# Performance work log

Hardware: AMD Instinct MI355X
Metric: run time of the kernel (lower is better)

Reference implementation:

```python
import jax, jax.numpy as jnp
import numpy as np

B, S, D = 8, 1024, 1024
H, DK, DV = 16, 64, 64
MAXREL = 32
VOCAB = 2 * MAXREL + 1  # use_neg_dist=True


def setup_inputs() -> dict:
    key = jax.random.key(0)
    ks = jax.random.split(key, 16)
    s = 0.02
    return {
        "key": jax.random.normal(ks[0], (B, S, D), jnp.float32),
        "value": jax.random.normal(ks[1], (B, S, D), jnp.float32),
        "query": jax.random.normal(ks[2], (B, S, D), jnp.float32),
        # True = masked (masked_fill semantics)
        "mask": jax.random.bernoulli(ks[3], 0.1, (B, S, S)),
        # adjacency weights in {0,1,2}; 0 => disconnected, >0 => 1/adj reweight
        "adj_mask": jax.random.randint(ks[4], (B, H, S, S), 0, 3).astype(jnp.float32),
        "Wq": jax.random.normal(ks[5], (D, H * DK), jnp.float32) * s,
        "bq": jnp.zeros((H * DK,), jnp.float32),
        "Wk": jax.random.normal(ks[6], (D, H * DK), jnp.float32) * s,
        "bk": jnp.zeros((H * DK,), jnp.float32),
        "Wv": jax.random.normal(ks[7], (D, H * DV), jnp.float32) * s,
        "bv": jnp.zeros((H * DV,), jnp.float32),
        "Wo": jax.random.normal(ks[8], (H * DV, D), jnp.float32) * s,
        "bo": jnp.zeros((D,), jnp.float32),
        "rel_k": jax.random.normal(ks[9], (VOCAB, DK), jnp.float32) * s,
        "rel_v": jax.random.normal(ks[10], (VOCAB, DV), jnp.float32) * s,
    }


def reference(key, value, query, mask, adj_mask, Wq, bq, Wk, bk, Wv, bv, Wo, bo, rel_k, rel_v):
    Bq, Sq, _ = query.shape
    # project and split heads -> [B, H, S, d]
    k = (key @ Wk + bk).reshape(Bq, -1, H, DK).transpose(0, 2, 1, 3)
    q = (query @ Wq + bq).reshape(Bq, -1, H, DK).transpose(0, 2, 1, 3)
    v = (value @ Wv + bv).reshape(Bq, -1, H, DV).transpose(0, 2, 1, 3)
    Sk = k.shape[2]
    # relative position matrix (clamped signed distances, shifted to [0, 2*MAXREL])
    r = jnp.arange(Sk)
    dist = jnp.clip(r[None, :] - r[:, None], -MAXREL, MAXREL) + MAXREL  # [S, S]
    rk = rel_k[dist]  # [S, S, DK]
    rv = rel_v[dist]  # [S, S, DV]
    q = q / jnp.sqrt(jnp.asarray(DK, q.dtype))
    # content scores + relative-key scores (relative_matmul transpose=True)
    scores = jnp.einsum("bhqd,bhkd->bhqk", q, k) + jnp.einsum("bhqd,qkd->bhqk", q, rk)
    scores = scores.astype(jnp.float32)
    scores = jnp.where(mask[:, None, :, :], -1e18, scores)
    adj_b = adj_mask != 0.0
    scores = jnp.where(adj_b, scores, -1e18)
    attn = jax.nn.softmax(scores, axis=-1).astype(q.dtype)
    # adjacency renormalization: attn / adj where adj>0, then L1 normalize
    inv_adj = 1.0 / jnp.where(adj_b, adj_mask, 1e18)
    attn = attn * inv_adj
    attn = attn / jnp.maximum(jnp.sum(jnp.abs(attn), axis=-1, keepdims=True), 1e-12)
    # context + relative-value term (relative_matmul transpose=False)
    ctx = jnp.einsum("bhqk,bhkd->bhqd", attn, v) + jnp.einsum("bhqk,qkd->bhqd", attn, rv)
    ctx = ctx.transpose(0, 2, 1, 3).reshape(Bq, Sq, H * DV)
    final_output = ctx @ Wo + bo
    return final_output, attn
```

## Files before the change

### kernel.cpp

```cpp
#include <hip/hip_runtime.h>

typedef unsigned short u16;
typedef unsigned int u32;
typedef __bf16 bf16x8 __attribute__((ext_vector_type(8)));
typedef u16 u16x8 __attribute__((ext_vector_type(8)));
typedef float floatx4 __attribute__((ext_vector_type(4)));

#define B_ 8
#define S_ 1024
#define D_ 1024
#define H_ 16
#define NREL 65

__device__ __forceinline__ float b2f(u16 u) { return __uint_as_float(((u32)u) << 16); }
__device__ __forceinline__ u16 f2b(float f) {
    u32 x = __float_as_uint(f);
    x += 0x7fffu + ((x >> 16) & 1u);
    return (u16)(x >> 16);
}

__global__ __launch_bounds__(256) void transpose_w(const float* __restrict__ in,
                                                   u16* __restrict__ out) {
    __shared__ u16 tile[32][33];
    int c0 = blockIdx.x * 32, r0 = blockIdx.y * 32;
    int tx = threadIdx.x & 31, ty = threadIdx.x >> 5;
#pragma unroll
    for (int i = 0; i < 32; i += 8)
        tile[ty + i][tx] = f2b(in[(size_t)(r0 + ty + i) * 1024 + c0 + tx]);
    __syncthreads();
#pragma unroll
    for (int i = 0; i < 32; i += 8)
        out[(size_t)(c0 + ty + i) * 1024 + r0 + tx] = tile[tx][ty + i];
}

__global__ __launch_bounds__(256) void transpose_v(const u16* __restrict__ in,
                                                   u16* __restrict__ out) {
    __shared__ u16 tile[32][33];
    int bh = blockIdx.z;
    int s0 = blockIdx.x * 32, d0 = blockIdx.y * 32;
    int tx = threadIdx.x & 31, ty = threadIdx.x >> 5;
    const u16* ib = in + (size_t)bh * S_ * 64;
    u16* ob = out + (size_t)bh * S_ * 64;
#pragma unroll
    for (int i = 0; i < 32; i += 8)
        tile[ty + i][tx] = ib[(size_t)(s0 + ty + i) * 64 + d0 + tx];
    __syncthreads();
#pragma unroll
    for (int i = 0; i < 32; i += 8)
        ob[(size_t)(d0 + ty + i) * 1024 + s0 + tx] = tile[tx][ty + i];
}

__global__ __launch_bounds__(256, 2) void gemm_bt(
    const void* __restrict__ Av, const u16* __restrict__ WT, const float* __restrict__ bias,
    float* __restrict__ outf, u16* __restrict__ outb, int M, int K, int mode, int a_bf16,
    float scale) {
    __shared__ __align__(16) u16 As[128 * 64];
    __shared__ __align__(16) u16 Bs[128 * 64];
    int tid = threadIdx.x;
    int wave = tid >> 6, lane = tid & 63;
    int wm = (wave >> 1) * 64, wn = (wave & 1) * 64;
    int m0 = blockIdx.y * 128, n0 = blockIdx.x * 128;
    floatx4 acc[4][4] = {};
    for (int kt = 0; kt < K; kt += 64) {
        if (a_bf16) {
            const u16* A = (const u16*)Av;
#pragma unroll
            for (int i = 0; i < 4; i++) {
                int L = tid + 256 * i;
                int row = L >> 3, seg = (L & 7) * 8;
                *(uint4*)(As + row * 64 + seg) = *(const uint4*)(A + (size_t)(m0 + row) * K + kt + seg);
            }
        } else {
            const float* A = (const float*)Av;
#pragma unroll
            for (int i = 0; i < 8; i++) {
                int L = tid + 256 * i;
                int row = L >> 4, seg = (L & 15) * 4;
                float4 a = *(const float4*)(A + (size_t)(m0 + row) * K + kt + seg);
                ushort4 b;
                b.x = f2b(a.x); b.y = f2b(a.y); b.z = f2b(a.z); b.w = f2b(a.w);
                *(ushort4*)(As + row * 64 + seg) = b;
            }
        }
#pragma unroll
        for (int i = 0; i < 4; i++) {
            int L = tid + 256 * i;
            int row = L >> 3, seg = (L & 7) * 8;
            *(uint4*)(Bs + row * 64 + seg) = *(const uint4*)(WT + (size_t)(n0 + row) * K + kt + seg);
        }
        __syncthreads();
        int kb = (lane >> 4) * 8;
#pragma unroll
        for (int half = 0; half < 2; half++) {
            bf16x8 af[4], bfv[4];
#pragma unroll
            for (int mi = 0; mi < 4; mi++)
                af[mi] = *(const bf16x8*)(As + (wm + mi * 16 + (lane & 15)) * 64 + half * 32 + kb);
#pragma unroll
            for (int ni = 0; ni < 4; ni++)
                bfv[ni] = *(const bf16x8*)(Bs + (wn + ni * 16 + (lane & 15)) * 64 + half * 32 + kb);
#pragma unroll
            for (int mi = 0; mi < 4; mi++)
#pragma unroll
                for (int ni = 0; ni < 4; ni++)
                    acc[mi][ni] = __builtin_amdgcn_mfma_f32_16x16x32_bf16(af[mi], bfv[ni], acc[mi][ni], 0, 0, 0);
        }
        __syncthreads();
    }
    int lr = (lane >> 4) * 4, lc = lane & 15;
#pragma unroll
    for (int mi = 0; mi < 4; mi++) {
#pragma unroll
        for (int ni = 0; ni < 4; ni++) {
            int col = n0 + wn + ni * 16 + lc;
            float bv = bias[col];
#pragma unroll
            for (int r = 0; r < 4; r++) {
                int row = m0 + wm + mi * 16 + lr + r;
                float v = (acc[mi][ni][r] + bv) * scale;
                if (mode == 0) {
                    outf[(size_t)row * 1024 + col] = v;
                } else {
                    int b = row >> 10, s = row & 1023;
                    int hh = col >> 6, d = col & 63;
                    outb[(((size_t)(b * H_ + hh)) * S_ + s) * 64 + d] = f2b(v);
                }
            }
        }
    }
}

__global__ __launch_bounds__(256, 2) void attn_fused(
    const u16* __restrict__ qw, const u16* __restrict__ kw, const u16* __restrict__ vt,
    const int* __restrict__ mask, const float* __restrict__ adj,
    const float* __restrict__ relk, const float* __restrict__ relv,
    float* __restrict__ attn_out, u16* __restrict__ ctx) {
    __shared__ __align__(16) u16 s_attn[16 * 1024];
    __shared__ float s_qrel[16 * NREL];
    __shared__ float s_arel[16 * NREL];
    __shared__ float s_redm[4 * 16];
    __shared__ float s_reds[4 * 16 * 2];

    const int tid = threadIdx.x;
    const int w = tid >> 6;
    const int lane = tid & 63;
    const int g = lane >> 4;
    const int li = lane & 15;
    const int q0 = blockIdx.x * 16;
    const int h = blockIdx.y, b = blockIdx.z;
    const size_t bh = (size_t)b * H_ + h;
    const u16* qb = qw + bh * S_ * 64;
    const u16* kb = kw + bh * S_ * 64;

    bf16x8 aq[2];
#pragma unroll
    for (int kf = 0; kf < 2; kf++)
        aq[kf] = *(const bf16x8*)(qb + (size_t)(q0 + li) * 64 + kf * 32 + g * 8);

    for (int ni = w; ni < 5; ni += 4) {
        floatx4 qacc = {};
        int v = ni * 16 + li;
        int vc = v > 64 ? 64 : v;
#pragma unroll
        for (int kf = 0; kf < 2; kf++) {
            const float* rp = relk + vc * 64 + kf * 32 + g * 8;
            float4 f0 = *(const float4*)(rp);
            float4 f1 = *(const float4*)(rp + 4);
            u16x8 t;
            t[0] = f2b(f0.x); t[1] = f2b(f0.y); t[2] = f2b(f0.z); t[3] = f2b(f0.w);
            t[4] = f2b(f1.x); t[5] = f2b(f1.y); t[6] = f2b(f1.z); t[7] = f2b(f1.w);
            qacc = __builtin_amdgcn_mfma_f32_16x16x32_bf16(aq[kf], *(bf16x8*)&t, qacc, 0, 0, 0);
        }
        if (v <= 64) {
#pragma unroll
            for (int r = 0; r < 4; r++) s_qrel[(g * 4 + r) * NREL + v] = qacc[r];
        }
    }
    __syncthreads();

    floatx4 acc[16] = {};
#pragma unroll
    for (int kf = 0; kf < 2; kf++) {
#pragma unroll
        for (int ni = 0; ni < 16; ni++) {
            int kcol = w * 256 + ni * 16 + li;
            bf16x8 bk = *(const bf16x8*)(kb + (size_t)kcol * 64 + kf * 32 + g * 8);
            acc[ni] = __builtin_amdgcn_mfma_f32_16x16x32_bf16(aq[kf], bk, acc[ni], 0, 0, 0);
        }
    }

    const int* mbase = mask + (size_t)b * S_ * S_;
    const float* abase = adj + bh * S_ * S_;
#pragma unroll
    for (int ni = 0; ni < 16; ni++) {
        int kcol = w * 256 + ni * 16 + li;
#pragma unroll
        for (int r = 0; r < 4; r++) {
            int qpos = q0 + g * 4 + r;
            int dd = kcol - qpos;
            dd = max(-32, min(32, dd));
            float sc = acc[ni][r] + s_qrel[(g * 4 + r) * NREL + dd + 32];
            int mk = mbase[(size_t)qpos * S_ + kcol];
            float aj = abase[(size_t)qpos * S_ + kcol];
            if (mk != 0 || aj == 0.f) sc = -1e18f;
            acc[ni][r] = sc;
        }
    }

    float mr[4];
#pragma unroll
    for (int r = 0; r < 4; r++) {
        float m = acc[0][r];
#pragma unroll
        for (int ni = 1; ni < 16; ni++) m = fmaxf(m, acc[ni][r]);
#pragma unroll
        for (int o = 8; o > 0; o >>= 1) m = fmaxf(m, __shfl_xor(m, o, 16));
        mr[r] = m;
    }
    if (li == 0) {
#pragma unroll
        for (int r = 0; r < 4; r++) s_redm[w * 16 + g * 4 + r] = mr[r];
    }
    __syncthreads();
#pragma unroll
    for (int r = 0; r < 4; r++) {
        float m = s_redm[g * 4 + r];
#pragma unroll
        for (int ww = 1; ww < 4; ww++) m = fmaxf(m, s_redm[ww * 16 + g * 4 + r]);
        mr[r] = m;
    }

    float psum[4] = {0.f, 0.f, 0.f, 0.f}, pisum[4] = {0.f, 0.f, 0.f, 0.f};
#pragma unroll
    for (int ni = 0; ni < 16; ni++) {
        int kcol = w * 256 + ni * 16 + li;
#pragma unroll
        for (int r = 0; r < 4; r++) {
            int qpos = q0 + g * 4 + r;
            float aj = abase[(size_t)qpos * S_ + kcol];
            float p = __expf(acc[ni][r] - mr[r]);
            float inv = (aj != 0.f) ? (1.f / aj) : 1e-18f;
            float pi = p * inv;
            acc[ni][r] = pi;
            psum[r] += p;
            pisum[r] += pi;
        }
    }
#pragma unroll
    for (int r = 0; r < 4; r++)
#pragma unroll
        for (int o = 8; o > 0; o >>= 1) {
            psum[r] += __shfl_xor(psum[r], o, 16);
            pisum[r] += __shfl_xor(pisum[r], o, 16);
        }
    if (li == 0) {
#pragma unroll
        for (int r = 0; r < 4; r++) {
            s_reds[(w * 16 + g * 4 + r) * 2 + 0] = psum[r];
            s_reds[(w * 16 + g * 4 + r) * 2 + 1] = pisum[r];
        }
    }
    __syncthreads();
    float rden[4];
#pragma unroll
    for (int r = 0; r < 4; r++) {
        float ps = 0.f, pis = 0.f;
#pragma unroll
        for (int ww = 0; ww < 4; ww++) {
            ps += s_reds[(ww * 16 + g * 4 + r) * 2 + 0];
            pis += s_reds[(ww * 16 + g * 4 + r) * 2 + 1];
        }
        rden[r] = 1.f / fmaxf(pis, 1e-12f * ps);
    }

    float* ob = attn_out + bh * (size_t)S_ * S_;
#pragma unroll
    for (int ni = 0; ni < 16; ni++) {
        int kcol = w * 256 + ni * 16 + li;
#pragma unroll
        for (int r = 0; r < 4; r++) {
            int row = g * 4 + r;
            float at = acc[ni][r] * rden[r];
            ob[(size_t)(q0 + row) * S_ + kcol] = at;
            int byteoff = (row * 2048 + kcol * 2) ^ ((row & 7) << 4);
            *(u16*)((char*)s_attn + byteoff) = f2b(at);
        }
    }
    __syncthreads();

    {
        const int row = tid >> 4, sub = tid & 15;
        const int qpos = q0 + row;
        auto rd = [&](int k) -> float {
            int byteoff = (row * 2048 + k * 2) ^ ((row & 7) << 4);
            return b2f(*(const u16*)((const char*)s_attn + byteoff));
        };
        float s0v = 0.f;
        for (int k = sub; k <= qpos - 32; k += 16) s0v += rd(k);
#pragma unroll
        for (int o = 8; o > 0; o >>= 1) s0v += __shfl_xor(s0v, o, 16);
        if (sub == 0) s_arel[row * NREL + 0] = s0v;
        float s1v = 0.f;
        for (int k = qpos + 32 + sub; k < S_; k += 16) s1v += rd(k);
#pragma unroll
        for (int o = 8; o > 0; o >>= 1) s1v += __shfl_xor(s1v, o, 16);
        if (sub == 0) s_arel[row * NREL + 64] = s1v;
        for (int i = sub; i < 63; i += 16) {
            int v = 1 + i;
            int k = qpos + v - 32;
            s_arel[row * NREL + v] = (k >= 0 && k < S_) ? rd(k) : 0.f;
        }
    }

    floatx4 pv = {};
    const int d = w * 16 + li;
    const u16* vrow = vt + (bh * 64 + d) * (size_t)S_;
#pragma unroll 8
    for (int kt = 0; kt < S_; kt += 32) {
        int byteoff = (li * 2048 + (kt + g * 8) * 2) ^ ((li & 7) << 4);
        bf16x8 pa = *(const bf16x8*)((const char*)s_attn + byteoff);
        bf16x8 vb8 = *(const bf16x8*)(vrow + kt + g * 8);
        pv = __builtin_amdgcn_mfma_f32_16x16x32_bf16(pa, vb8, pv, 0, 0, 0);
    }
    __syncthreads();

#pragma unroll 1
    for (int v = 0; v < NREL; v++) {
        float rv = relv[v * 64 + d];
#pragma unroll
        for (int r = 0; r < 4; r++) pv[r] += s_arel[(g * 4 + r) * NREL + v] * rv;
    }
    u16* cb = ctx + ((size_t)b * S_ + q0) * 1024 + h * 64 + d;
#pragma unroll
    for (int r = 0; r < 4; r++) cb[(size_t)(g * 4 + r) * 1024] = f2b(pv[r]);
}

extern "C" void kernel_launch(void* const* d_in, const int* in_sizes, int n_in,
                              void* d_out, int out_size, void* d_ws, size_t ws_size,
                              hipStream_t stream) {
    const float* key   = (const float*)d_in[0];
    const float* value = (const float*)d_in[1];
    const float* query = (const float*)d_in[2];
    const int* mask    = (const int*)d_in[3];
    const float* adj   = (const float*)d_in[4];
    const float* Wq = (const float*)d_in[5];  const float* bq = (const float*)d_in[6];
    const float* Wk = (const float*)d_in[7];  const float* bk = (const float*)d_in[8];
    const float* Wv = (const float*)d_in[9];  const float* bv = (const float*)d_in[10];
    const float* Wo = (const float*)d_in[11]; const float* bo = (const float*)d_in[12];
    const float* relk = (const float*)d_in[13];
    const float* relv = (const float*)d_in[14];

    float* out_final = (float*)d_out;
    float* out_attn  = out_final + (size_t)B_ * S_ * D_;

    char* ws = (char*)d_ws;
    u16* wt  = (u16*)ws;
    u16* qws = (u16*)(ws + ((size_t)2 << 20));
    u16* kws = (u16*)(ws + ((size_t)18 << 20));
    u16* vws = (u16*)(ws + ((size_t)34 << 20));
    u16* vtw = (u16*)(ws + ((size_t)50 << 20));
    u16* cws = (u16*)(ws + ((size_t)66 << 20));

    dim3 tg(32, 32), tb(256);
    dim3 gg(8, 64), gb(256);
    dim3 vg(32, 2, 128), vb_(256);
    dim3 ag(64, 16, 8), ab(256);

    transpose_w<<<tg, tb, 0, stream>>>(Wq, wt);
    gemm_bt<<<gg, gb, 0, stream>>>(query, wt, bq, nullptr, qws, 8192, 1024, 1, 0, 0.125f);
    transpose_w<<<tg, tb, 0, stream>>>(Wk, wt);
    gemm_bt<<<gg, gb, 0, stream>>>(key, wt, bk, nullptr, kws, 8192, 1024, 1, 0, 1.0f);
    transpose_w<<<tg, tb, 0, stream>>>(Wv, wt);
    gemm_bt<<<gg, gb, 0, stream>>>(value, wt, bv, nullptr, vws, 8192, 1024, 1, 0, 1.0f);
    transpose_v<<<vg, vb_, 0, stream>>>(vws, vtw);
    attn_fused<<<ag, ab, 0, stream>>>(qws, kws, vtw, mask, adj, relk, relv, out_attn, cws);
    transpose_w<<<tg, tb, 0, stream>>>(Wo, wt);
    gemm_bt<<<gg, gb, 0, stream>>>(cws, wt, bo, out_final, nullptr, 8192, 1024, 0, 1, 1.0f);
}
```

Baseline: 2.220 ms.

## Batch weight transposes and QKV GEMMs, cache adj in LDS, raise attention occupancy

All four weight transposes now run in one launch, and the three Q/K/V projection GEMMs run in one launch via blockIdx.z, which cuts launch count and fills more of the GPU. The attention kernel stages adj values as bf16 in LDS so the second pass no longer re-reads adj from global memory. It also merges the two 65-wide shared arrays into one, copies relv into LDS before the relative-value loop, and raises launch_bounds to 4 blocks per CU. Risks: rounding adj to bf16 could change the 1/adj values (though {0,1,2} are exact), and the higher occupancy target may cause register spills.

```diff
diff --git a/kernel.cpp b/kernel.cpp
--- a/kernel.cpp
+++ b/kernel.cpp
@@ -19,9 +19,14 @@
     return (u16)(x >> 16);
 }
 
-__global__ __launch_bounds__(256) void transpose_w(const float* __restrict__ in,
-                                                   u16* __restrict__ out) {
+__global__ __launch_bounds__(256) void transpose_w4(
+    const float* __restrict__ w0, const float* __restrict__ w1,
+    const float* __restrict__ w2, const float* __restrict__ w3,
+    u16* __restrict__ out) {
     __shared__ u16 tile[32][33];
+    int z = blockIdx.z;
+    const float* in = (z == 0) ? w0 : (z == 1) ? w1 : (z == 2) ? w2 : w3;
+    u16* o = out + (size_t)z * 1024 * 1024;
     int c0 = blockIdx.x * 32, r0 = blockIdx.y * 32;
     int tx = threadIdx.x & 31, ty = threadIdx.x >> 5;
 #pragma unroll
@@ -30,7 +35,7 @@
     __syncthreads();
 #pragma unroll
     for (int i = 0; i < 32; i += 8)
-        out[(size_t)(c0 + ty + i) * 1024 + r0 + tx] = tile[tx][ty + i];
+        o[(size_t)(c0 + ty + i) * 1024 + r0 + tx] = tile[tx][ty + i];
 }
 
 __global__ __launch_bounds__(256) void transpose_v(const u16* __restrict__ in,
@@ -50,10 +55,81 @@
         ob[(size_t)(d0 + ty + i) * 1024 + s0 + tx] = tile[tx][ty + i];
 }
 
+__global__ __launch_bounds__(256, 2) void gemm_qkv(
+    const float* __restrict__ Aq, const float* __restrict__ Ak, const float* __restrict__ Avv,
+    const u16* __restrict__ wt4, const float* __restrict__ bq, const float* __restrict__ bk,
+    const float* __restrict__ bv, u16* __restrict__ oq, u16* __restrict__ ok,
+    u16* __restrict__ ov) {
+    __shared__ __align__(16) u16 As[128 * 64];
+    __shared__ __align__(16) u16 Bs[128 * 64];
+    int z = blockIdx.z;
+    const float* A = (z == 0) ? Aq : (z == 1) ? Ak : Avv;
+    const u16* WT = wt4 + (size_t)z * 1024 * 1024;
+    const float* bias = (z == 0) ? bq : (z == 1) ? bk : bv;
+    u16* outb = (z == 0) ? oq : (z == 1) ? ok : ov;
+    float scale = (z == 0) ? 0.125f : 1.0f;
+    int tid = threadIdx.x;
+    int wave = tid >> 6, lane = tid & 63;
+    int wm = (wave >> 1) * 64, wn = (wave & 1) * 64;
+    int m0 = blockIdx.y * 128, n0 = blockIdx.x * 128;
+    floatx4 acc[4][4] = {};
+    for (int kt = 0; kt < 1024; kt += 64) {
+#pragma unroll
+        for (int i = 0; i < 8; i++) {
+            int L = tid + 256 * i;
+            int row = L >> 4, seg = (L & 15) * 4;
+            float4 a = *(const float4*)(A + (size_t)(m0 + row) * 1024 + kt + seg);
+            ushort4 bb;
+            bb.x = f2b(a.x); bb.y = f2b(a.y); bb.z = f2b(a.z); bb.w = f2b(a.w);
+            *(ushort4*)(As + row * 64 + seg) = bb;
+        }
+#pragma unroll
+        for (int i = 0; i < 4; i++) {
+            int L = tid + 256 * i;
+            int row = L >> 3, seg = (L & 7) * 8;
+            *(uint4*)(Bs + row * 64 + seg) = *(const uint4*)(WT + (size_t)(n0 + row) * 1024 + kt + seg);
+        }
+        __syncthreads();
+        int kb = (lane >> 4) * 8;
+#pragma unroll
+        for (int half = 0; half < 2; half++) {
+            bf16x8 af[4], bfv[4];
+#pragma unroll
+            for (int mi = 0; mi < 4; mi++)
+                af[mi] = *(const bf16x8*)(As + (wm + mi * 16 + (lane & 15)) * 64 + half * 32 + kb);
+#pragma unroll
+            for (int ni = 0; ni < 4; ni++)
+                bfv[ni] = *(const bf16x8*)(Bs + (wn + ni * 16 + (lane & 15)) * 64 + half * 32 + kb);
+#pragma unroll
+            for (int mi = 0; mi < 4; mi++)
+#pragma unroll
+                for (int ni = 0; ni < 4; ni++)
+                    acc[mi][ni] = __builtin_amdgcn_mfma_f32_16x16x32_bf16(af[mi], bfv[ni], acc[mi][ni], 0, 0, 0);
+        }
+        __syncthreads();
+    }
+    int lr = (lane >> 4) * 4, lc = lane & 15;
+#pragma unroll
+    for (int mi = 0; mi < 4; mi++) {
+#pragma unroll
+        for (int ni = 0; ni < 4; ni++) {
+            int col = n0 + wn + ni * 16 + lc;
+            float bvv = bias[col];
+#pragma unroll
+            for (int r = 0; r < 4; r++) {
+                int row = m0 + wm + mi * 16 + lr + r;
+                float v = (acc[mi][ni][r] + bvv) * scale;
+                int b = row >> 10, s = row & 1023;
+                int hh = col >> 6, d = col & 63;
+                outb[(((size_t)(b * H_ + hh)) * S_ + s) * 64 + d] = f2b(v);
+            }
+        }
+    }
+}
+
 __global__ __launch_bounds__(256, 2) void gemm_bt(
-    const void* __restrict__ Av, const u16* __restrict__ WT, const float* __restrict__ bias,
-    float* __restrict__ outf, u16* __restrict__ outb, int M, int K, int mode, int a_bf16,
-    float scale) {
+    const u16* __restrict__ A, const u16* __restrict__ WT, const float* __restrict__ bias,
+    float* __restrict__ outf) {
     __shared__ __align__(16) u16 As[128 * 64];
     __shared__ __align__(16) u16 Bs[128 * 64];
     int tid = threadIdx.x;
@@ -61,32 +137,18 @@
     int wm = (wave >> 1) * 64, wn = (wave & 1) * 64;
     int m0 = blockIdx.y * 128, n0 = blockIdx.x * 128;
     floatx4 acc[4][4] = {};
-    for (int kt = 0; kt < K; kt += 64) {
-        if (a_bf16) {
-            const u16* A = (const u16*)Av;
-#pragma unroll
-            for (int i = 0; i < 4; i++) {
-                int L = tid + 256 * i;
-                int row = L >> 3, seg = (L & 7) * 8;
-                *(uint4*)(As + row * 64 + seg) = *(const uint4*)(A + (size_t)(m0 + row) * K + kt + seg);
-            }
-        } else {
-            const float* A = (const float*)Av;
-#pragma unroll
-            for (int i = 0; i < 8; i++) {
-                int L = tid + 256 * i;
-                int row = L >> 4, seg = (L & 15) * 4;
-                float4 a = *(const float4*)(A + (size_t)(m0 + row) * K + kt + seg);
-                ushort4 b;
-                b.x = f2b(a.x); b.y = f2b(a.y); b.z = f2b(a.z); b.w = f2b(a.w);
-                *(ushort4*)(As + row * 64 + seg) = b;
-            }
-        }
+    for (int kt = 0; kt < 1024; kt += 64) {
 #pragma unroll
         for (int i = 0; i < 4; i++) {
             int L = tid + 256 * i;
             int row = L >> 3, seg = (L & 7) * 8;
-            *(uint4*)(Bs + row * 64 + seg) = *(const uint4*)(WT + (size_t)(n0 + row) * K + kt + seg);
+            *(uint4*)(As + row * 64 + seg) = *(const uint4*)(A + (size_t)(m0 + row) * 1024 + kt + seg);
+        }
+#pragma unroll
+        for (int i = 0; i < 4; i++) {
+            int L = tid + 256 * i;
+            int row = L >> 3, seg = (L & 7) * 8;
+            *(uint4*)(Bs + row * 64 + seg) = *(const uint4*)(WT + (size_t)(n0 + row) * 1024 + kt + seg);
         }
         __syncthreads();
         int kb = (lane >> 4) * 8;
@@ -113,33 +175,25 @@
 #pragma unroll
         for (int ni = 0; ni < 4; ni++) {
             int col = n0 + wn + ni * 16 + lc;
-            float bv = bias[col];
+            float bvv = bias[col];
 #pragma unroll
             for (int r = 0; r < 4; r++) {
                 int row = m0 + wm + mi * 16 + lr + r;
-                float v = (acc[mi][ni][r] + bv) * scale;
-                if (mode == 0) {
-                    outf[(size_t)row * 1024 + col] = v;
-                } else {
-                    int b = row >> 10, s = row & 1023;
-                    int hh = col >> 6, d = col & 63;
-                    outb[(((size_t)(b * H_ + hh)) * S_ + s) * 64 + d] = f2b(v);
-                }
+                outf[(size_t)row * 1024 + col] = acc[mi][ni][r] + bvv;
             }
         }
     }
 }
 
-__global__ __launch_bounds__(256, 2) void attn_fused(
+__global__ __launch_bounds__(256, 4) void attn_fused(
     const u16* __restrict__ qw, const u16* __restrict__ kw, const u16* __restrict__ vt,
     const int* __restrict__ mask, const float* __restrict__ adj,
     const float* __restrict__ relk, const float* __restrict__ relv,
     float* __restrict__ attn_out, u16* __restrict__ ctx) {
     __shared__ __align__(16) u16 s_attn[16 * 1024];
-    __shared__ float s_qrel[16 * NREL];
-    __shared__ float s_arel[16 * NREL];
-    __shared__ float s_redm[4 * 16];
-    __shared__ float s_reds[4 * 16 * 2];
+    __shared__ __align__(16) float s_q65[16 * NREL];
+    __shared__ float s_redm[64];
+    __shared__ float s_reds[128];
 
     const int tid = threadIdx.x;
     const int w = tid >> 6;
@@ -173,7 +227,7 @@
         }
         if (v <= 64) {
 #pragma unroll
-            for (int r = 0; r < 4; r++) s_qrel[(g * 4 + r) * NREL + v] = qacc[r];
+            for (int r = 0; r < 4; r++) s_q65[(g * 4 + r) * NREL + v] = qacc[r];
         }
     }
     __syncthreads();
@@ -196,12 +250,14 @@
         int kcol = w * 256 + ni * 16 + li;
 #pragma unroll
         for (int r = 0; r < 4; r++) {
-            int qpos = q0 + g * 4 + r;
+            int row = g * 4 + r;
+            int qpos = q0 + row;
             int dd = kcol - qpos;
             dd = max(-32, min(32, dd));
-            float sc = acc[ni][r] + s_qrel[(g * 4 + r) * NREL + dd + 32];
+            float sc = acc[ni][r] + s_q65[row * NREL + dd + 32];
             int mk = mbase[(size_t)qpos * S_ + kcol];
             float aj = abase[(size_t)qpos * S_ + kcol];
+            *(u16*)((char*)s_attn + ((row * 2048 + kcol * 2) ^ ((row & 7) << 4))) = f2b(aj);
             if (mk != 0 || aj == 0.f) sc = -1e18f;
             acc[ni][r] = sc;
         }
@@ -236,8 +292,8 @@
         int kcol = w * 256 + ni * 16 + li;
 #pragma unroll
         for (int r = 0; r < 4; r++) {
-            int qpos = q0 + g * 4 + r;
-            float aj = abase[(size_t)qpos * S_ + kcol];
+            int row = g * 4 + r;
+            float aj = b2f(*(const u16*)((const char*)s_attn + ((row * 2048 + kcol * 2) ^ ((row & 7) << 4))));
             float p = __expf(acc[ni][r] - mr[r]);
             float inv = (aj != 0.f) ? (1.f / aj) : 1e-18f;
             float pi = p * inv;
@@ -282,8 +338,7 @@
             int row = g * 4 + r;
             float at = acc[ni][r] * rden[r];
             ob[(size_t)(q0 + row) * S_ + kcol] = at;
-            int byteoff = (row * 2048 + kcol * 2) ^ ((row & 7) << 4);
-            *(u16*)((char*)s_attn + byteoff) = f2b(at);
+            *(u16*)((char*)s_attn + ((row * 2048 + kcol * 2) ^ ((row & 7) << 4))) = f2b(at);
         }
     }
     __syncthreads();
@@ -299,16 +354,16 @@
         for (int k = sub; k <= qpos - 32; k += 16) s0v += rd(k);
 #pragma unroll
         for (int o = 8; o > 0; o >>= 1) s0v += __shfl_xor(s0v, o, 16);
-        if (sub == 0) s_arel[row * NREL + 0] = s0v;
+        if (sub == 0) s_q65[row * NREL + 0] = s0v;
         float s1v = 0.f;
         for (int k = qpos + 32 + sub; k < S_; k += 16) s1v += rd(k);
 #pragma unroll
         for (int o = 8; o > 0; o >>= 1) s1v += __shfl_xor(s1v, o, 16);
-        if (sub == 0) s_arel[row * NREL + 64] = s1v;
+        if (sub == 0) s_q65[row * NREL + 64] = s1v;
         for (int i = sub; i < 63; i += 16) {
             int v = 1 + i;
             int k = qpos + v - 32;
-            s_arel[row * NREL + v] = (k >= 0 && k < S_) ? rd(k) : 0.f;
+            s_q65[row * NREL + v] = (k >= 0 && k < S_) ? rd(k) : 0.f;
         }
     }
 
@@ -324,11 +379,18 @@
     }
     __syncthreads();
 
-#pragma unroll 1
+    float* s_rv = (float*)s_attn;
+    {
+        float4* dst = (float4*)s_rv;
+        const float4* src = (const float4*)relv;
+        for (int i = tid; i < NREL * 16; i += 256) dst[i] = src[i];
+    }
+    __syncthreads();
+#pragma unroll 4
     for (int v = 0; v < NREL; v++) {
-        float rv = relv[v * 64 + d];
-#pragma unroll
-        for (int r = 0; r < 4; r++) pv[r] += s_arel[(g * 4 + r) * NREL + v] * rv;
+        float rv = s_rv[v * 64 + d];
+#pragma unroll
+        for (int r = 0; r < 4; r++) pv[r] += s_q65[(g * 4 + r) * NREL + v] * rv;
     }
     u16* cb = ctx + ((size_t)b * S_ + q0) * 1024 + h * 64 + d;
 #pragma unroll
@@ -354,26 +416,23 @@
     float* out_attn  = out_final + (size_t)B_ * S_ * D_;
 
     char* ws = (char*)d_ws;
-    u16* wt  = (u16*)ws;
-    u16* qws = (u16*)(ws + ((size_t)2 << 20));
-    u16* kws = (u16*)(ws + ((size_t)18 << 20));
-    u16* vws = (u16*)(ws + ((size_t)34 << 20));
-    u16* vtw = (u16*)(ws + ((size_t)50 << 20));
-    u16* cws = (u16*)(ws + ((size_t)66 << 20));
-
-    dim3 tg(32, 32), tb(256);
-    dim3 gg(8, 64), gb(256);
-    dim3 vg(32, 2, 128), vb_(256);
-    dim3 ag(64, 16, 8), ab(256);
-
-    transpose_w<<<tg, tb, 0, stream>>>(Wq, wt);
-    gemm_bt<<<gg, gb, 0, stream>>>(query, wt, bq, nullptr, qws, 8192, 1024, 1, 0, 0.125f);
-    transpose_w<<<tg, tb, 0, stream>>>(Wk, wt);
-    gemm_bt<<<gg, gb, 0, stream>>>(key, wt, bk, nullptr, kws, 8192, 1024, 1, 0, 1.0f);
-    transpose_w<<<tg, tb, 0, stream>>>(Wv, wt);
-    gemm_bt<<<gg, gb, 0, stream>>>(value, wt, bv, nullptr, vws, 8192, 1024, 1, 0, 1.0f);
-    transpose_v<<<vg, vb_, 0, stream>>>(vws, vtw);
-    attn_fused<<<ag, ab, 0, stream>>>(qws, kws, vtw, mask, adj, relk, relv, out_attn, cws);
-    transpose_w<<<tg, tb, 0, stream>>>(Wo, wt);
-    gemm_bt<<<gg, gb, 0, stream>>>(cws, wt, bo, out_final, nullptr, 8192, 1024, 0, 1, 1.0f);
-}
+    u16* wt4 = (u16*)ws;
+    u16* qws = (u16*)(ws + ((size_t)8 << 20));
+    u16* kws = (u16*)(ws + ((size_t)24 << 20));
+    u16* vtw = (u16*)(ws + ((size_t)40 << 20));
+    u16* cws = (u16*)(ws + ((size_t)56 << 20));
+    u16* vws = cws;
+
+    dim3 tb(256);
+    dim3 t4g(32, 32, 4);
+    dim3 qkvg(8, 64, 3);
+    dim3 vg(32, 2, 128);
+    dim3 ag(64, 16, 8);
+    dim3 gg(8, 64);
+
+    transpose_w4<<<t4g, tb, 0, stream>>>(Wq, Wk, Wv, Wo, wt4);
+    gemm_qkv<<<qkvg, tb, 0, stream>>>(query, key, value, wt4, bq, bk, bv, qws, kws, vws);
+    transpose_v<<<vg, tb, 0, stream>>>(vws, vtw);
+    attn_fused<<<ag, tb, 0, stream>>>(qws, kws, vtw, mask, adj, relk, relv, out_attn, cws);
+    gemm_bt<<<gg, tb, 0, stream>>>(cws, wt4 + (size_t)3 * 1024 * 1024, bo, out_final);
+}
```

New measurement: 2.003 ms. -9.8%, faster.
